# Optimization experiments

Measured on AMD Instinct MI355X. Metric: run time of the kernel, lower is better.

Reference implementation:

```python
import jax, jax.numpy as jnp
import numpy as np

ANGLE_BINS = 16
RADIUS_BINS = 8


def _bilinear_cart(img, ys, xs):
    # img [B,C,H,W]; ys/xs: sample grid [A,R] in pixel coords, zero outside image
    h, w = img.shape[2], img.shape[3]
    y0 = jnp.floor(ys)
    x0 = jnp.floor(xs)
    wy = (ys - y0).astype(img.dtype)
    wx = (xs - x0).astype(img.dtype)
    y0i = jnp.clip(y0, 0, h - 1).astype(jnp.int32)
    y1i = jnp.clip(y0 + 1, 0, h - 1).astype(jnp.int32)
    x0i = jnp.clip(x0, 0, w - 1).astype(jnp.int32)
    x1i = jnp.clip(x0 + 1, 0, w - 1).astype(jnp.int32)
    v00 = img[:, :, y0i, x0i]
    v01 = img[:, :, y0i, x1i]
    v10 = img[:, :, y1i, x0i]
    v11 = img[:, :, y1i, x1i]
    out = (v00 * (1 - wy) * (1 - wx) + v01 * (1 - wy) * wx
           + v10 * wy * (1 - wx) + v11 * wy * wx)
    valid = ((ys >= 0) & (ys <= h - 1) & (xs >= 0) & (xs <= w - 1)).astype(img.dtype)
    return out * valid


def cartesian_to_polar(x):
    # [B,C,H,W] -> [B,C,ANGLE_BINS,RADIUS_BINS] via bilinear sampling on a polar grid
    b, c, h, w = x.shape
    cy = (h - 1) / 2.0
    cx = (w - 1) / 2.0
    max_r = min(h, w) / 2.0
    theta = 2.0 * jnp.pi * jnp.arange(ANGLE_BINS, dtype=jnp.float32) / ANGLE_BINS
    r = (jnp.arange(RADIUS_BINS, dtype=jnp.float32) + 0.5) / RADIUS_BINS * max_r
    ys = cy + r[None, :] * jnp.sin(theta)[:, None]  # [A,R]
    xs = cx + r[None, :] * jnp.cos(theta)[:, None]  # [A,R]
    return _bilinear_cart(x, ys, xs)


def polar_to_cartesian(pf, h, w):
    # [B,C,A,R] -> [B,C,H,W]: inverse remap with angular wrap, radial clamp,
    # zero outside the max radius disc
    b, c, A, R = pf.shape
    cy = (h - 1) / 2.0
    cx = (w - 1) / 2.0
    max_r = min(h, w) / 2.0
    yy, xx = jnp.meshgrid(jnp.arange(h, dtype=jnp.float32),
                          jnp.arange(w, dtype=jnp.float32), indexing='ij')
    dy = yy - cy
    dx = xx - cx
    rr = jnp.sqrt(dy * dy + dx * dx)
    th = jnp.mod(jnp.arctan2(dy, dx), 2.0 * jnp.pi)
    a = th / (2.0 * jnp.pi) * A
    ri = rr / max_r * R - 0.5
    a0 = jnp.floor(a)
    wa = (a - a0).astype(pf.dtype)
    a0i = jnp.mod(a0.astype(jnp.int32), A)
    a1i = jnp.mod(a0i + 1, A)
    r0 = jnp.floor(ri)
    wr = (ri - r0).astype(pf.dtype)
    r0i = jnp.clip(r0, 0, R - 1).astype(jnp.int32)
    r1i = jnp.clip(r0 + 1, 0, R - 1).astype(jnp.int32)
    v00 = pf[:, :, a0i, r0i]
    v01 = pf[:, :, a0i, r1i]
    v10 = pf[:, :, a1i, r0i]
    v11 = pf[:, :, a1i, r1i]
    out = (v00 * (1 - wa) * (1 - wr) + v01 * (1 - wa) * wr
           + v10 * wa * (1 - wr) + v11 * wa * wr)
    valid = (rr <= max_r).astype(pf.dtype)
    return out * valid


def setup_inputs() -> dict:
    key = jax.random.key(0)
    ks = jax.random.split(key, 4)
    B, C, H, W = 16, 256, 128, 128
    x = jax.random.normal(ks[0], (B, C, H, W), dtype=jnp.float32)
    # grouped 3x3 conv: groups=4 -> kernel [C_out=C, C_in/groups=C//4, 3, 3]
    w_polar = jax.random.normal(ks[1], (C, C // 4, 3, 3), dtype=jnp.float32) * 0.05
    b_polar = jnp.zeros((C,), jnp.float32)
    w_attn1 = jax.random.normal(ks[2], (C // 4, C), dtype=jnp.float32) * 0.05
    b_attn1 = jnp.zeros((C // 4,), jnp.float32)
    w_attn2 = jax.random.normal(ks[3], (1, C // 4), dtype=jnp.float32) * 0.05
    b_attn2 = jnp.zeros((1,), jnp.float32)
    return {"x": x, "w_polar": w_polar, "b_polar": b_polar,
            "w_attn1": w_attn1, "b_attn1": b_attn1,
            "w_attn2": w_attn2, "b_attn2": b_attn2}


def reference(x, w_polar, b_polar, w_attn1, b_attn1, w_attn2, b_attn2):
    b, c, h, w = x.shape
    pf = cartesian_to_polar(x)  # [B,C,16,8]
    pp = jax.lax.conv_general_dilated(
        pf, w_polar, window_strides=(1, 1), padding=((1, 1), (1, 1)),
        dimension_numbers=('NCHW', 'OIHW', 'NCHW'), feature_group_count=4)
    pp = pp + b_polar[None, :, None, None]
    pc = polar_to_cartesian(pp, h, w)  # [B,C,H,W]
    h1 = jax.nn.relu(jnp.einsum('bchw,oc->bohw', pc, w_attn1)
                     + b_attn1[None, :, None, None])
    att = jax.nn.sigmoid(jnp.einsum('bchw,oc->bohw', h1, w_attn2)
                         + b_attn2[None, :, None, None])  # [B,1,H,W]
    return x * att
```

## Files before the change

### kernel.cpp

```cpp
#include <hip/hip_runtime.h>
#include <math.h>

#define TWO_PI 6.28318530717958647692f

typedef float f4 __attribute__((ext_vector_type(4)));

__global__ __launch_bounds__(256) void k1_cart2polar(const float* __restrict__ x,
                                                     float* __restrict__ pf) {
    __shared__ float w00s[128], w01s[128], w10s[128], w11s[128];
    __shared__ int   o00s[128], o01s[128], o10s[128], o11s[128];
    int tid = threadIdx.x;
    if (tid < 128) {
        int a = tid >> 3, r = tid & 7;
        float theta = (TWO_PI * (float)a) / 16.0f;
        float rad   = ((float)r + 0.5f) / 8.0f * 64.0f;
        float ys = 63.5f + rad * sinf(theta);
        float xs = 63.5f + rad * cosf(theta);
        float y0 = floorf(ys), x0 = floorf(xs);
        float wy = ys - y0,    wx = xs - x0;
        int y0i = min(max((int)y0, 0), 127);
        int y1i = min(max((int)y0 + 1, 0), 127);
        int x0i = min(max((int)x0, 0), 127);
        int x1i = min(max((int)x0 + 1, 0), 127);
        float valid = (ys >= 0.0f && ys <= 127.0f && xs >= 0.0f && xs <= 127.0f) ? 1.0f : 0.0f;
        w00s[tid] = valid * (1.0f - wy) * (1.0f - wx);
        w01s[tid] = valid * (1.0f - wy) * wx;
        w10s[tid] = valid * wy * (1.0f - wx);
        w11s[tid] = valid * wy * wx;
        o00s[tid] = y0i * 128 + x0i;
        o01s[tid] = y0i * 128 + x1i;
        o10s[tid] = y1i * 128 + x0i;
        o11s[tid] = y1i * 128 + x1i;
    }
    __syncthreads();
    int t = blockIdx.x * 256 + tid;
    int bin = t & 127;
    int img = t >> 7;
    const float* ib = x + ((size_t)img << 14);
    float v = ib[o00s[bin]] * w00s[bin]
            + ib[o01s[bin]] * w01s[bin]
            + ib[o10s[bin]] * w10s[bin]
            + ib[o11s[bin]] * w11s[bin];
    pf[t] = v;
}

__global__ __launch_bounds__(256) void k2_conv(const float* __restrict__ pf,
                                               const float* __restrict__ w_polar,
                                               const float* __restrict__ b_polar,
                                               float* __restrict__ pp_t) {
    __shared__ __align__(16) float pfs[64 * 180];
    __shared__ __align__(16) float red[128 * 8];
    int bid = blockIdx.x;
    int b  = bid >> 5;
    int g  = (bid >> 3) & 3;
    int ot = bid & 7;
    int tid = threadIdx.x;
    for (int i = tid; i < 64 * 180; i += 256) pfs[i] = 0.0f;
    __syncthreads();
    const float* src = pf + ((size_t)(b * 256 + g * 64) << 7);
    for (int i = tid; i < 8192; i += 256) {
        int ic = i >> 7, bin = i & 127;
        pfs[ic * 180 + ((bin >> 3) + 1) * 10 + (bin & 7) + 1] = src[i];
    }
    __syncthreads();

    int half = tid >> 7;
    int bt   = tid & 127;
    int a = bt >> 3, r = bt & 7;
    int oc0 = g * 64 + ot * 8;
    float acc[8];
    #pragma unroll
    for (int j = 0; j < 8; ++j) acc[j] = 0.0f;

    const float* wbase = w_polar + (size_t)oc0 * 576 + half * 288;
    const float* pbase = pfs + half * 32 * 180 + a * 10 + r;
    for (int ic = 0; ic < 32; ++ic) {
        float v[9];
        const float* base = pbase + ic * 180;
        #pragma unroll
        for (int dh = 0; dh < 3; ++dh)
            #pragma unroll
            for (int dw = 0; dw < 3; ++dw)
                v[dh * 3 + dw] = base[dh * 10 + dw];
        #pragma unroll
        for (int j = 0; j < 8; ++j) {
            const float* wp = wbase + j * 576 + ic * 9;
            acc[j] += wp[0]*v[0] + wp[1]*v[1] + wp[2]*v[2]
                    + wp[3]*v[3] + wp[4]*v[4] + wp[5]*v[5]
                    + wp[6]*v[6] + wp[7]*v[7] + wp[8]*v[8];
        }
    }
    if (half) {
        #pragma unroll
        for (int j = 0; j < 8; ++j) red[bt * 8 + j] = acc[j];
    }
    __syncthreads();
    if (!half) {
        float* dst = pp_t + ((size_t)((b << 7) + bt)) * 256 + oc0;
        #pragma unroll
        for (int j = 0; j < 8; ++j)
            dst[j] = acc[j] + red[bt * 8 + j] + b_polar[oc0 + j];
    }
}

__global__ __launch_bounds__(256) void k3_proj(const float* __restrict__ pp_t,
                                               const float* __restrict__ w_attn1,
                                               float* __restrict__ q) {
    __shared__ __align__(16) float wl[16384];
    int tid = threadIdx.x;
    for (int i = tid; i < 16384; i += 256) {
        int o = i >> 8, c = i & 255;
        wl[(c << 6) + (o ^ (c & 31))] = w_attn1[i];
    }
    __syncthreads();
    int n = blockIdx.x * 256 + tid;
    int b   = n >> 13;
    int bin = (n >> 6) & 127;
    int o   = n & 63;
    const float4* pr4 = (const float4*)(pp_t + ((size_t)((b << 7) + bin)) * 256);
    float acc = 0.0f;
    #pragma unroll 8
    for (int c4 = 0; c4 < 64; ++c4) {
        float4 p = pr4[c4];
        int c = c4 << 2;
        acc += wl[( c      << 6) + (o ^ ( c      & 31))] * p.x;
        acc += wl[((c + 1) << 6) + (o ^ ((c + 1) & 31))] * p.y;
        acc += wl[((c + 2) << 6) + (o ^ ((c + 2) & 31))] * p.z;
        acc += wl[((c + 3) << 6) + (o ^ ((c + 3) & 31))] * p.w;
    }
    q[n] = acc;
}

__global__ __launch_bounds__(256) void k4a_att(const float* __restrict__ q,
                                               const float* __restrict__ b_attn1,
                                               const float* __restrict__ w_attn2,
                                               const float* __restrict__ b_attn2,
                                               float* __restrict__ att) {
    __shared__ __align__(16) float qs[8896];
    __shared__ __align__(16) float b1s[64];
    __shared__ __align__(16) float w2s[64];
    int b    = blockIdx.x >> 6;
    int tile = blockIdx.x & 63;
    int tid  = threadIdx.x;
    const float* qb = q + ((size_t)b << 13);
    for (int i = tid; i < 8192; i += 256) {
        int bin = i >> 6, o = i & 63;
        qs[(bin >> 3) * 556 + (bin & 7) * 68 + o] = qb[i];
    }
    if (tid < 64) { b1s[tid] = b_attn1[tid]; w2s[tid] = w_attn2[tid]; }
    __syncthreads();
    float b2 = b_attn2[0];
    const float4* q4  = (const float4*)qs;
    const float4* b14 = (const float4*)b1s;
    const float4* w24 = (const float4*)w2s;

    int p = (tile << 8) + tid;
    int h = p >> 7, w = p & 127;
    float dy = (float)h - 63.5f;
    float dx = (float)w - 63.5f;
    float rr = sqrtf(dy * dy + dx * dx);
    float th = atan2f(dy, dx);
    if (th < 0.0f) th += TWO_PI;
    float aa = th / TWO_PI * 16.0f;
    float a0 = floorf(aa);
    float wa = aa - a0;
    int ia0 = ((int)a0) & 15;
    int ia1 = (ia0 + 1) & 15;
    float ri = rr / 64.0f * 8.0f - 0.5f;
    float r0 = floorf(ri);
    float wr = ri - r0;
    int ir0 = (int)fminf(fmaxf(r0, 0.0f), 7.0f);
    int ir1 = (int)fminf(fmaxf(r0 + 1.0f, 0.0f), 7.0f);
    float valid = (rr <= 64.0f) ? 1.0f : 0.0f;
    float w00 = valid * (1.0f - wa) * (1.0f - wr);
    float w01 = valid * (1.0f - wa) * wr;
    float w10 = valid * wa * (1.0f - wr);
    float w11 = valid * wa * wr;
    int t00 = ia0 * 139 + ir0 * 17;
    int t01 = ia0 * 139 + ir1 * 17;
    int t10 = ia1 * 139 + ir0 * 17;
    int t11 = ia1 * 139 + ir1 * 17;
    float acc = b2;
    #pragma unroll
    for (int i = 0; i < 16; ++i) {
        float4 v00 = q4[t00 + i], v01 = q4[t01 + i];
        float4 v10 = q4[t10 + i], v11 = q4[t11 + i];
        float4 bb = b14[i], ww = w24[i];
        float sx = w00 * v00.x + w01 * v01.x + w10 * v10.x + w11 * v11.x;
        float sy = w00 * v00.y + w01 * v01.y + w10 * v10.y + w11 * v11.y;
        float sz = w00 * v00.z + w01 * v01.z + w10 * v10.z + w11 * v11.z;
        float sw = w00 * v00.w + w01 * v01.w + w10 * v10.w + w11 * v11.w;
        acc += fmaxf(sx + bb.x, 0.0f) * ww.x;
        acc += fmaxf(sy + bb.y, 0.0f) * ww.y;
        acc += fmaxf(sz + bb.z, 0.0f) * ww.z;
        acc += fmaxf(sw + bb.w, 0.0f) * ww.w;
    }
    float attv = 1.0f / (1.0f + __expf(-acc));
    att[((size_t)b << 14) + p] = attv;
}

__global__ __launch_bounds__(256) void k4b_mul(const f4* __restrict__ x4,
                                               const float* __restrict__ att,
                                               f4* __restrict__ out4) {
    const f4* att4 = (const f4*)att;
    int idx = blockIdx.x * 256 + threadIdx.x;
    int stride = gridDim.x * 256;
    for (int i = idx; i < 16777216; i += stride) {
        f4 xv = __builtin_nontemporal_load(&x4[i]);
        f4 av = att4[((i >> 20) << 12) | (i & 4095)];
        __builtin_nontemporal_store(xv * av, &out4[i]);
    }
}

extern "C" void kernel_launch(void* const* d_in, const int* in_sizes, int n_in,
                              void* d_out, int out_size, void* d_ws, size_t ws_size,
                              hipStream_t stream) {
    const float* x       = (const float*)d_in[0];
    const float* w_polar = (const float*)d_in[1];
    const float* b_polar = (const float*)d_in[2];
    const float* w_attn1 = (const float*)d_in[3];
    const float* b_attn1 = (const float*)d_in[4];
    const float* w_attn2 = (const float*)d_in[5];
    const float* b_attn2 = (const float*)d_in[6];
    float* out = (float*)d_out;
    float* ws  = (float*)d_ws;

    float* pf   = ws;
    float* pp_t = ws + 524288;
    float* q    = ws + 1048576;
    float* att  = ws + 1179648;

    hipLaunchKernelGGL(k1_cart2polar, dim3(2048), dim3(256), 0, stream, x, pf);
    hipLaunchKernelGGL(k2_conv,       dim3(512),  dim3(256), 0, stream, pf, w_polar, b_polar, pp_t);
    hipLaunchKernelGGL(k3_proj,       dim3(512),  dim3(256), 0, stream, pp_t, w_attn1, q);
    hipLaunchKernelGGL(k4a_att,       dim3(1024), dim3(256), 0, stream, q, b_attn1, w_attn2, b_attn2, att);
    hipLaunchKernelGGL(k4b_mul,       dim3(2048), dim3(256), 0, stream,
                       (const f4*)x, att, (f4*)out);
}
```

Baseline: 172.0 us.

## Stage conv weights in LDS and split input channels into two passes

The grouped polar convolution kernel now uses 128 threads per block. Instead of two thread halves each taking 32 input channels and reducing through shared memory, each block loops over two passes of 32 channels. In each pass the block stages those channels plus a transposed weight tile in LDS, and reads the weights as float4 vectors broadcast across lanes. This removes the per-thread scattered global weight loads and the cross-half reduction. In exchange it halves the threads per block and adds an extra pair of barriers and a serial second pass.

```diff
diff --git a/kernel.cpp b/kernel.cpp
--- a/kernel.cpp
+++ b/kernel.cpp
@@ -44,63 +44,67 @@
     pf[t] = v;
 }
 
-__global__ __launch_bounds__(256) void k2_conv(const float* __restrict__ pf,
+__global__ __launch_bounds__(128) void k2_conv(const float* __restrict__ pf,
                                                const float* __restrict__ w_polar,
                                                const float* __restrict__ b_polar,
                                                float* __restrict__ pp_t) {
-    __shared__ __align__(16) float pfs[64 * 180];
-    __shared__ __align__(16) float red[128 * 8];
+    __shared__ __align__(16) float pfs[32 * 180];
+    __shared__ __align__(16) float wls[32 * 72];
     int bid = blockIdx.x;
     int b  = bid >> 5;
     int g  = (bid >> 3) & 3;
     int ot = bid & 7;
     int tid = threadIdx.x;
-    for (int i = tid; i < 64 * 180; i += 256) pfs[i] = 0.0f;
-    __syncthreads();
-    const float* src = pf + ((size_t)(b * 256 + g * 64) << 7);
-    for (int i = tid; i < 8192; i += 256) {
-        int ic = i >> 7, bin = i & 127;
-        pfs[ic * 180 + ((bin >> 3) + 1) * 10 + (bin & 7) + 1] = src[i];
-    }
-    __syncthreads();
-
-    int half = tid >> 7;
-    int bt   = tid & 127;
-    int a = bt >> 3, r = bt & 7;
+    int a = tid >> 3, r = tid & 7;
     int oc0 = g * 64 + ot * 8;
+
+    for (int i = tid; i < 32 * 180; i += 128) pfs[i] = 0.0f;
+    __syncthreads();
+
     float acc[8];
     #pragma unroll
     for (int j = 0; j < 8; ++j) acc[j] = 0.0f;
-
-    const float* wbase = w_polar + (size_t)oc0 * 576 + half * 288;
-    const float* pbase = pfs + half * 32 * 180 + a * 10 + r;
-    for (int ic = 0; ic < 32; ++ic) {
-        float v[9];
-        const float* base = pbase + ic * 180;
-        #pragma unroll
-        for (int dh = 0; dh < 3; ++dh)
+    const float* src = pf + ((size_t)(b * 256 + g * 64) << 7);
+
+    for (int pass = 0; pass < 2; ++pass) {
+        for (int i = tid; i < 4096; i += 128) {
+            int icl = i >> 7, bin = i & 127;
+            pfs[icl * 180 + ((bin >> 3) + 1) * 10 + (bin & 7) + 1]
+                = src[pass * 4096 + i];
+        }
+        for (int i = tid; i < 2304; i += 128) {
+            int icl = i / 72, rem = i - icl * 72;
+            int tap = rem >> 3, j = rem & 7;
+            wls[i] = w_polar[(size_t)(oc0 + j) * 576 + (pass * 32 + icl) * 9 + tap];
+        }
+        __syncthreads();
+
+        const float* pbase = pfs + a * 10 + r;
+        for (int ic = 0; ic < 32; ++ic) {
+            float v[9];
+            const float* base = pbase + ic * 180;
             #pragma unroll
-            for (int dw = 0; dw < 3; ++dw)
-                v[dh * 3 + dw] = base[dh * 10 + dw];
-        #pragma unroll
-        for (int j = 0; j < 8; ++j) {
-            const float* wp = wbase + j * 576 + ic * 9;
-            acc[j] += wp[0]*v[0] + wp[1]*v[1] + wp[2]*v[2]
-                    + wp[3]*v[3] + wp[4]*v[4] + wp[5]*v[5]
-                    + wp[6]*v[6] + wp[7]*v[7] + wp[8]*v[8];
+            for (int dh = 0; dh < 3; ++dh)
+                #pragma unroll
+                for (int dw = 0; dw < 3; ++dw)
+                    v[dh * 3 + dw] = base[dh * 10 + dw];
+            const f4* wrow = (const f4*)(wls + ic * 72);
+            #pragma unroll
+            for (int tap = 0; tap < 9; ++tap) {
+                f4 wlo = wrow[tap * 2];
+                f4 whi = wrow[tap * 2 + 1];
+                float vt = v[tap];
+                acc[0] += wlo.x * vt;  acc[1] += wlo.y * vt;
+                acc[2] += wlo.z * vt;  acc[3] += wlo.w * vt;
+                acc[4] += whi.x * vt;  acc[5] += whi.y * vt;
+                acc[6] += whi.z * vt;  acc[7] += whi.w * vt;
+            }
         }
-    }
-    if (half) {
-        #pragma unroll
-        for (int j = 0; j < 8; ++j) red[bt * 8 + j] = acc[j];
-    }
-    __syncthreads();
-    if (!half) {
-        float* dst = pp_t + ((size_t)((b << 7) + bt)) * 256 + oc0;
-        #pragma unroll
-        for (int j = 0; j < 8; ++j)
-            dst[j] = acc[j] + red[bt * 8 + j] + b_polar[oc0 + j];
-    }
+        __syncthreads();
+    }
+    float* dst = pp_t + ((size_t)(b * 128 + tid)) * 256 + oc0;
+    #pragma unroll
+    for (int j = 0; j < 8; ++j) dst[j] = acc[j] + b_polar[oc0 + j];
 }
 
 __global__ __launch_bounds__(256) void k3_proj(const float* __restrict__ pp_t,
@@ -231,9 +235,11 @@
     float* att  = ws + 1179648;
 
     hipLaunchKernelGGL(k1_cart2polar, dim3(2048), dim3(256), 0, stream, x, pf);
-    hipLaunchKernelGGL(k2_conv,       dim3(512),  dim3(256), 0, stream, pf, w_polar, b_polar, pp_t);
+    hipLaunchKernelGGL(k2_conv,       dim3(512),  dim3(128), 0, stream,
+                       pf, w_polar, b_polar, pp_t);
     hipLaunchKernelGGL(k3_proj,       dim3(512),  dim3(256), 0, stream, pp_t, w_attn1, q);
-    hipLaunchKernelGGL(k4a_att,       dim3(1024), dim3(256), 0, stream, q, b_attn1, w_attn2, b_attn2, att);
+    hipLaunchKernelGGL(k4a_att,       dim3(1024), dim3(256), 0, stream,
+                       q, b_attn1, w_attn2, b_attn2, att);
     hipLaunchKernelGGL(k4b_mul,       dim3(2048), dim3(256), 0, stream,
                        (const f4*)x, att, (f4*)out);
 }
```

Result: faster. 160.6 us (-6.6%).
